# Kernel tuning notes

Hardware: AMD Instinct MI355X
Metric: run time of the kernel (lower is better)

The kernel has to match this reference:

```python
import jax, jax.numpy as jnp
import numpy as np

BSZ, L, H, P = 8, 4096, 512, 256  # batch, seq len, features, complex state dim (conj_sym)
DT_MIN, DT_MAX = 1e-3, 1e-1


def setup_inputs() -> dict:
    key = jax.random.key(0)
    k_u, k_B, k_C, k_D, k_dt = jax.random.split(key, 5)
    u = jax.random.normal(k_u, (BSZ, L, H), dtype=jnp.float32)
    # HiPPO-like stable init for the diagonal state matrix
    Lambda_re = -0.5 * jnp.ones((P,), dtype=jnp.float32)
    Lambda_im = jnp.pi * jnp.arange(P, dtype=jnp.float32)
    # lecun-normal-ish scaling for real/imag parts of B (fan_in = H) and C (fan_in = P)
    B = jax.random.normal(k_B, (P, H, 2), dtype=jnp.float32) / jnp.sqrt(2.0 * H)
    C = jax.random.normal(k_C, (H, P, 2), dtype=jnp.float32) / jnp.sqrt(2.0 * P)
    D = jax.random.normal(k_D, (H,), dtype=jnp.float32)
    log_step = jax.random.uniform(k_dt, (P, 1), dtype=jnp.float32,
                                  minval=jnp.log(DT_MIN), maxval=jnp.log(DT_MAX))
    return {"u": u, "Lambda_re": Lambda_re, "Lambda_im": Lambda_im,
            "B": B, "C": C, "D": D, "log_step": log_step}


def _binop(q_i, q_j):
    """Associative binary operator for diagonal linear recurrence."""
    A_i, b_i = q_i
    A_j, b_j = q_j
    return (A_j * A_i, A_j * b_i + b_j)


def reference(u, Lambda_re, Lambda_im, B, C, D, log_step):
    # --- setup / discretization (zero-order hold) ---
    Lambda = (Lambda_re + 1j * Lambda_im).astype(jnp.complex64)      # (P,)
    B_tilde = (B[..., 0] + 1j * B[..., 1]).astype(jnp.complex64)     # (P,H)
    C_tilde = (C[..., 0] + 1j * C[..., 1]).astype(jnp.complex64)     # (H,P)
    step = jnp.exp(log_step[:, 0])                                   # (P,)
    Lambda_bar = jnp.exp(Lambda * step)                              # (P,)
    B_bar = ((Lambda_bar - 1.0) / Lambda)[:, None] * B_tilde         # (P,H)

    # --- parallel scan over the sequence (diagonal SSM) ---
    Bu = jnp.einsum('blh,ph->blp', u, B_bar)                         # (B,L,P) complex64
    Lam = jnp.broadcast_to(Lambda_bar, Bu.shape)                     # (B,L,P)
    _, xs = jax.lax.associative_scan(_binop, (Lam, Bu), axis=1)      # (B,L,P)

    # --- emissions (factor 2 from conjugate symmetry) + feedthrough ---
    ys = 2.0 * jnp.einsum('blp,hp->blh', xs, C_tilde).real + D * u   # (B,L,H)
    return jax.nn.gelu(ys)
```

## Files before the change

kernel.cpp:

```cpp
#include <hip/hip_runtime.h>
#include <cstdint>
#include <cstddef>

typedef unsigned short u16;
typedef short short8 __attribute__((ext_vector_type(8)));
typedef float floatx4 __attribute__((ext_vector_type(4)));

#define DEVINL __device__ __forceinline__

static constexpr int BSZ = 8, SEQL = 4096, H = 512, P = 256;
static constexpr int M = BSZ * SEQL;
static constexpr int KD = 512;
static constexpr int ND = 512;
static constexpr int CHUNK = 32;
static constexpr int NCH = SEQL / CHUNK;

DEVINL u16 f2bf(float f) {
  union { float f; unsigned u; } v; v.f = f;
  unsigned r = (v.u + 0x7fffu + ((v.u >> 16) & 1u)) >> 16;
  return (u16)r;
}
DEVINL float bf2f(u16 h) {
  union { unsigned u; float f; } v; v.u = ((unsigned)h) << 16; return v.f;
}

DEVINL void gload_lds16(const u16* g, u16* l) {
  __builtin_amdgcn_global_load_lds(
      (const __attribute__((address_space(1))) unsigned*)g,
      (__attribute__((address_space(3))) unsigned*)l, 16, 0, 0);
}

__global__ void setup_kernel(const float* __restrict__ Lre, const float* __restrict__ Lim,
                             const float* __restrict__ logstep,
                             float2* __restrict__ lam, float2* __restrict__ ffac) {
  int p = threadIdx.x;
  if (p >= P) return;
  float lr = Lre[p], li = Lim[p];
  float st = expf(logstep[p]);
  float mag = expf(lr * st);
  float ang = li * st;
  float cr = mag * cosf(ang);
  float ci = mag * sinf(ang);
  lam[p] = make_float2(cr, ci);
  float a = cr - 1.0f, b = ci;
  float den = lr * lr + li * li;
  float fr = (a * lr + b * li) / den;
  float fi = (b * lr - a * li) / den;
  ffac[p] = make_float2(fr, fi);
}

__global__ void bt1_kernel(const float2* __restrict__ Bin,
                           const float2* __restrict__ ffac,
                           u16* __restrict__ bt1) {
  int idx = blockIdx.x * 256 + threadIdx.x;
  int p = idx / H, h = idx % H;
  float2 bv = Bin[(size_t)p * H + h];
  float2 f = ffac[p];
  float br = f.x * bv.x - f.y * bv.y;
  float bi = f.x * bv.y + f.y * bv.x;
  bt1[(size_t)(2 * p) * H + h]     = f2bf(br);
  bt1[(size_t)(2 * p + 1) * H + h] = f2bf(bi);
}

__global__ void bt2_kernel(const float* __restrict__ Cin, u16* __restrict__ bt2) {
  int idx = blockIdx.x * 256 + threadIdx.x;
  float c = Cin[idx];
  float v = (idx & 1) ? -2.0f * c : 2.0f * c;
  bt2[idx] = f2bf(v);
}

__global__ void ucvt_kernel(const float4* __restrict__ uin, ushort4* __restrict__ ubf) {
  int idx = blockIdx.x * 256 + threadIdx.x;
  float4 f = uin[idx];
  ushort4 o;
  o.x = f2bf(f.x); o.y = f2bf(f.y); o.z = f2bf(f.z); o.w = f2bf(f.w);
  ubf[idx] = o;
}

template <int MODE>
__global__ __launch_bounds__(256, 2) void gemm_bt(const u16* __restrict__ A,
                                                  const u16* __restrict__ Bt,
                                                  u16* __restrict__ outBf,
                                                  float* __restrict__ outF,
                                                  const float* __restrict__ Dv,
                                                  const u16* __restrict__ ubf) {
  __shared__ u16 As[3][128 * 32];
  __shared__ u16 Bs[3][256 * 32];
  const int tid = threadIdx.x;

  const int hw = blockIdx.x;
  const int logical = (hw & 7) * 64 + (hw >> 3);
  const int bm = logical >> 1;
  const int bn = logical & 1;

  const int wave = tid >> 6, lane = tid & 63;
  const int quad = lane >> 4, l16 = lane & 15;
  const int wm = (wave & 1) << 6;
  const int wn = (wave >> 1) << 7;

  floatx4 acc[4][8] = {};

  const u16* Ab = A + (size_t)bm * 128 * KD;
  const u16* Bb = Bt + (size_t)bn * 256 * KD;
  const int srow = tid >> 2;
  const int scol = (tid & 3) << 3;

#define STAGE(buf, kofs)                                                                   \
  do {                                                                                     \
    gload_lds16(Ab + (size_t)srow * KD + (kofs) + scol,         &As[buf][tid * 8]);        \
    gload_lds16(Ab + (size_t)(srow + 64) * KD + (kofs) + scol,  &As[buf][2048 + tid * 8]); \
    gload_lds16(Bb + (size_t)srow * KD + (kofs) + scol,         &Bs[buf][tid * 8]);        \
    gload_lds16(Bb + (size_t)(srow + 64) * KD + (kofs) + scol,  &Bs[buf][2048 + tid * 8]); \
    gload_lds16(Bb + (size_t)(srow + 128) * KD + (kofs) + scol, &Bs[buf][4096 + tid * 8]); \
    gload_lds16(Bb + (size_t)(srow + 192) * KD + (kofs) + scol, &Bs[buf][6144 + tid * 8]); \
  } while (0)

  STAGE(0, 0);
  STAGE(1, 32);
  asm volatile("s_waitcnt vmcnt(6)" ::: "memory");
  __builtin_amdgcn_sched_barrier(0);
  __builtin_amdgcn_s_barrier();
  __builtin_amdgcn_sched_barrier(0);

  constexpr int NK = KD / 32;
#pragma unroll
  for (int ks = 0; ks < NK; ks++) {
    const int k0 = ks * 32;
    const int cur = ks % 3;

    if (ks + 2 < NK) STAGE((ks + 2) % 3, k0 + 64);

    short8 af[4], bfr[8];
#pragma unroll
    for (int t = 0; t < 4; t++)
      af[t] = *(const short8*)&As[cur][(wm + t * 16 + l16) * 32 + quad * 8];
#pragma unroll
    for (int t = 0; t < 8; t++)
      bfr[t] = *(const short8*)&Bs[cur][(wn + t * 16 + l16) * 32 + quad * 8];

    asm volatile("s_waitcnt lgkmcnt(0)" ::: "memory");
    __builtin_amdgcn_sched_barrier(0);

    __builtin_amdgcn_s_setprio(1);
#pragma unroll
    for (int tm = 0; tm < 4; tm++)
#pragma unroll
      for (int tn = 0; tn < 8; tn++)
        acc[tm][tn] = __builtin_amdgcn_mfma_f32_16x16x32_bf16(af[tm], bfr[tn], acc[tm][tn], 0, 0, 0);
    __builtin_amdgcn_s_setprio(0);

    if (ks + 2 < NK) {
      asm volatile("s_waitcnt vmcnt(6)" ::: "memory");
      __builtin_amdgcn_sched_barrier(0);
      __builtin_amdgcn_s_barrier();
      __builtin_amdgcn_sched_barrier(0);
    } else if (ks + 1 < NK) {
      asm volatile("s_waitcnt vmcnt(0)" ::: "memory");
      __builtin_amdgcn_sched_barrier(0);
      __builtin_amdgcn_s_barrier();
      __builtin_amdgcn_sched_barrier(0);
    }
  }
#undef STAGE

  const int row_base = bm * 128 + wm + quad * 4;
  const int col_base = bn * 256 + wn + l16;
  float dv[8];
  if (MODE == 1) {
#pragma unroll
    for (int tn = 0; tn < 8; tn++) dv[tn] = Dv[col_base + tn * 16];
  }
#pragma unroll
  for (int tm = 0; tm < 4; tm++) {
#pragma unroll
    for (int tn = 0; tn < 8; tn++) {
      int n = col_base + tn * 16;
#pragma unroll
      for (int r = 0; r < 4; r++) {
        int m = row_base + tm * 16 + r;
        float v = acc[tm][tn][r];
        if (MODE == 0) {
          outBf[(size_t)m * ND + n] = f2bf(v);
        } else {
          float uv = bf2f(ubf[(size_t)m * ND + n]);
          float ys = v + dv[tn] * uv;
          float zz = ys + 0.044715f * (ys * ys * ys);
          float e = __builtin_amdgcn_exp2f(-2.3022082f * zz);
          outF[(size_t)m * ND + n] = ys * __builtin_amdgcn_rcpf(1.0f + e);
        }
      }
    }
  }
}

__global__ __launch_bounds__(256) void scan_carry(const u16* __restrict__ Bu,
                                                  const float2* __restrict__ lam,
                                                  float2* __restrict__ carry) {
  int p = threadIdx.x;
  int c = blockIdx.x;
  int b = blockIdx.y;
  float2 lm = lam[p];
  float xr = 0.f, xi = 0.f;
  const u16* base = Bu + ((size_t)b * SEQL + (size_t)c * CHUNK) * 512 + 2 * p;
  for (int l = 0; l < CHUNK; l++) {
    unsigned w = *(const unsigned*)(base + (size_t)l * 512);
    float br = bf2f((u16)(w & 0xffffu));
    float bi = bf2f((u16)(w >> 16));
    float nr = lm.x * xr - lm.y * xi + br;
    float ni = lm.x * xi + lm.y * xr + bi;
    xr = nr; xi = ni;
  }
  carry[((size_t)b * NCH + c) * P + p] = make_float2(xr, xi);
}

__global__ __launch_bounds__(256) void scan_prefix(const float2* __restrict__ carry,
                                                   const float2* __restrict__ lam,
                                                   float2* __restrict__ prefix) {
  int p = threadIdx.x;
  int b = blockIdx.x;
  float2 lm = lam[p];
  float ar = lm.x, ai = lm.y;
  for (int i = 0; i < 5; i++) { float nr = ar * ar - ai * ai, ni = 2.f * ar * ai; ar = nr; ai = ni; }
  float pr = 0.f, pi = 0.f;
  for (int c = 0; c < NCH; c++) {
    prefix[((size_t)b * NCH + c) * P + p] = make_float2(pr, pi);
    float2 ca = carry[((size_t)b * NCH + c) * P + p];
    float nr = ar * pr - ai * pi + ca.x;
    float ni = ar * pi + ai * pr + ca.y;
    pr = nr; pi = ni;
  }
}

__global__ __launch_bounds__(256) void scan_apply(u16* __restrict__ Bu,
                                                  const float2* __restrict__ lam,
                                                  const float2* __restrict__ prefix) {
  int p = threadIdx.x;
  int c = blockIdx.x;
  int b = blockIdx.y;
  float2 lm = lam[p];
  float2 pf = prefix[((size_t)b * NCH + c) * P + p];
  float xr = pf.x, xi = pf.y;
  u16* base = Bu + ((size_t)b * SEQL + (size_t)c * CHUNK) * 512 + 2 * p;
  for (int l = 0; l < CHUNK; l++) {
    unsigned* addr = (unsigned*)(base + (size_t)l * 512);
    unsigned w = *addr;
    float br = bf2f((u16)(w & 0xffffu));
    float bi = bf2f((u16)(w >> 16));
    float nr = lm.x * xr - lm.y * xi + br;
    float ni = lm.x * xi + lm.y * xr + bi;
    xr = nr; xi = ni;
    *addr = (unsigned)f2bf(nr) | ((unsigned)f2bf(ni) << 16);
  }
}

extern "C" void kernel_launch(void* const* d_in, const int* in_sizes, int n_in,
                              void* d_out, int out_size, void* d_ws, size_t ws_size,
                              hipStream_t stream) {
  const float* u      = (const float*)d_in[0];
  const float* Lre    = (const float*)d_in[1];
  const float* Lim    = (const float*)d_in[2];
  const float* Bin    = (const float*)d_in[3];
  const float* Cin    = (const float*)d_in[4];
  const float* Dv     = (const float*)d_in[5];
  const float* lstep  = (const float*)d_in[6];
  float* out          = (float*)d_out;

  char* ws = (char*)d_ws;
  float2* lam    = (float2*)(ws + 0);
  float2* ffac   = (float2*)(ws + 2048);
  u16*    bt1    = (u16*)   (ws + 4096);
  u16*    bt2    = (u16*)   (ws + 528384);
  u16*    ubf    = (u16*)   (ws + 1052672);
  u16*    Bu     = (u16*)   (ws + 34607104);
  float2* carry  = (float2*)(ws + 68161536);
  float2* prefix = (float2*)(ws + 69210112);

  setup_kernel<<<1, 256, 0, stream>>>(Lre, Lim, lstep, lam, ffac);
  bt1_kernel<<<(P * H) / 256, 256, 0, stream>>>((const float2*)Bin, ffac, bt1);
  bt2_kernel<<<(H * P * 2) / 256, 256, 0, stream>>>(Cin, bt2);
  ucvt_kernel<<<(M * H / 4) / 256, 256, 0, stream>>>((const float4*)u, (ushort4*)ubf);

  gemm_bt<0><<<(M / 128) * (ND / 256), 256, 0, stream>>>(ubf, bt1, Bu, nullptr, nullptr, nullptr);

  scan_carry <<<dim3(NCH, BSZ), 256, 0, stream>>>(Bu, lam, carry);
  scan_prefix<<<BSZ, 256, 0, stream>>>(carry, lam, prefix);
  scan_apply <<<dim3(NCH, BSZ), 256, 0, stream>>>(Bu, lam, prefix);

  gemm_bt<1><<<(M / 128) * (ND / 256), 256, 0, stream>>>(Bu, bt2, nullptr, out, Dv, ubf);
}
```

Measured before the change: 205.7 us.

## Fuse fp32-to-bf16 conversion into GEMM A-load and merge scan prefix into apply

The first GEMM now reads fp32 u directly into registers, converts to bf16 and writes to LDS, which removes the separate ucvt kernel and its bf16 workspace round trip. The second GEMM reads fp32 u for the feedthrough term instead of the bf16 copy. The scan_prefix kernel is removed: each scan_apply block recomputes its chunk prefix serially from the carries. That trades one small launch for redundant work that grows with chunk index, up to 128 steps. The register-staged A path adds VGPR pressure and doubles the A global traffic bytes inside the GEMM.

```diff
diff --git a/kernel.cpp b/kernel.cpp
--- a/kernel.cpp
+++ b/kernel.cpp
@@ -69,21 +69,14 @@
   bt2[idx] = f2bf(v);
 }
 
-__global__ void ucvt_kernel(const float4* __restrict__ uin, ushort4* __restrict__ ubf) {
-  int idx = blockIdx.x * 256 + threadIdx.x;
-  float4 f = uin[idx];
-  ushort4 o;
-  o.x = f2bf(f.x); o.y = f2bf(f.y); o.z = f2bf(f.z); o.w = f2bf(f.w);
-  ubf[idx] = o;
-}
-
 template <int MODE>
 __global__ __launch_bounds__(256, 2) void gemm_bt(const u16* __restrict__ A,
+                                                  const float* __restrict__ Af32,
                                                   const u16* __restrict__ Bt,
                                                   u16* __restrict__ outBf,
                                                   float* __restrict__ outF,
                                                   const float* __restrict__ Dv,
-                                                  const u16* __restrict__ ubf) {
+                                                  const float* __restrict__ U32) {
   __shared__ u16 As[3][128 * 32];
   __shared__ u16 Bs[3][256 * 32];
   const int tid = threadIdx.x;
@@ -100,35 +93,96 @@
 
   floatx4 acc[4][8] = {};
 
-  const u16* Ab = A + (size_t)bm * 128 * KD;
-  const u16* Bb = Bt + (size_t)bn * 256 * KD;
+  const u16*   Ab  = (MODE == 0) ? nullptr : A + (size_t)bm * 128 * KD;
+  const float* Afb = (MODE == 0) ? Af32 + (size_t)bm * 128 * KD : nullptr;
+  const u16*   Bb  = Bt + (size_t)bn * 256 * KD;
   const int srow = tid >> 2;
   const int scol = (tid & 3) << 3;
 
-#define STAGE(buf, kofs)                                                                   \
+  float4 aR[2][4];
+
+#define STAGE_B(buf, kofs)                                                                 \
   do {                                                                                     \
-    gload_lds16(Ab + (size_t)srow * KD + (kofs) + scol,         &As[buf][tid * 8]);        \
-    gload_lds16(Ab + (size_t)(srow + 64) * KD + (kofs) + scol,  &As[buf][2048 + tid * 8]); \
     gload_lds16(Bb + (size_t)srow * KD + (kofs) + scol,         &Bs[buf][tid * 8]);        \
     gload_lds16(Bb + (size_t)(srow + 64) * KD + (kofs) + scol,  &Bs[buf][2048 + tid * 8]); \
     gload_lds16(Bb + (size_t)(srow + 128) * KD + (kofs) + scol, &Bs[buf][4096 + tid * 8]); \
     gload_lds16(Bb + (size_t)(srow + 192) * KD + (kofs) + scol, &Bs[buf][6144 + tid * 8]); \
   } while (0)
 
-  STAGE(0, 0);
-  STAGE(1, 32);
-  asm volatile("s_waitcnt vmcnt(6)" ::: "memory");
-  __builtin_amdgcn_sched_barrier(0);
-  __builtin_amdgcn_s_barrier();
-  __builtin_amdgcn_sched_barrier(0);
+#define STAGE_A_LDS(buf, kofs)                                                             \
+  do {                                                                                     \
+    gload_lds16(Ab + (size_t)srow * KD + (kofs) + scol,        &As[buf][tid * 8]);         \
+    gload_lds16(Ab + (size_t)(srow + 64) * KD + (kofs) + scol, &As[buf][2048 + tid * 8]);  \
+  } while (0)
+
+#define ISSUE_A(set, kofs)                                                                 \
+  do {                                                                                     \
+    aR[set][0] = *(const float4*)(Afb + (size_t)srow * KD + (kofs) + scol);                \
+    aR[set][1] = *(const float4*)(Afb + (size_t)srow * KD + (kofs) + scol + 4);            \
+    aR[set][2] = *(const float4*)(Afb + (size_t)(srow + 64) * KD + (kofs) + scol);         \
+    aR[set][3] = *(const float4*)(Afb + (size_t)(srow + 64) * KD + (kofs) + scol + 4);     \
+  } while (0)
+
+#define WRITE_A(set, buf)                                                                  \
+  do {                                                                                     \
+    short8 w0, w1;                                                                         \
+    w0[0] = (short)f2bf(aR[set][0].x); w0[1] = (short)f2bf(aR[set][0].y);                  \
+    w0[2] = (short)f2bf(aR[set][0].z); w0[3] = (short)f2bf(aR[set][0].w);                  \
+    w0[4] = (short)f2bf(aR[set][1].x); w0[5] = (short)f2bf(aR[set][1].y);                  \
+    w0[6] = (short)f2bf(aR[set][1].z); w0[7] = (short)f2bf(aR[set][1].w);                  \
+    w1[0] = (short)f2bf(aR[set][2].x); w1[1] = (short)f2bf(aR[set][2].y);                  \
+    w1[2] = (short)f2bf(aR[set][2].z); w1[3] = (short)f2bf(aR[set][2].w);                  \
+    w1[4] = (short)f2bf(aR[set][3].x); w1[5] = (short)f2bf(aR[set][3].y);                  \
+    w1[6] = (short)f2bf(aR[set][3].z); w1[7] = (short)f2bf(aR[set][3].w);                  \
+    *(short8*)&As[buf][tid * 8]        = w0;                                               \
+    *(short8*)&As[buf][2048 + tid * 8] = w1;                                               \
+  } while (0)
+
+#define VMW(n) asm volatile("s_waitcnt vmcnt(" #n ")" ::: "memory");                       \
+               __builtin_amdgcn_sched_barrier(0)
+#define LGKW   asm volatile("s_waitcnt lgkmcnt(0)" ::: "memory");                          \
+               __builtin_amdgcn_sched_barrier(0)
+#define BARR   __builtin_amdgcn_s_barrier();                                               \
+               __builtin_amdgcn_sched_barrier(0)
 
   constexpr int NK = KD / 32;
+
+  if constexpr (MODE == 0) {
+    ISSUE_A(0, 0);
+    STAGE_B(0, 0);
+    ISSUE_A(1, 32);
+    STAGE_B(1, 32);
+    VMW(12);
+    WRITE_A(0, 0);
+    VMW(8);
+    LGKW;
+    BARR;
+  } else {
+    STAGE_A_LDS(0, 0);
+    STAGE_B(0, 0);
+    STAGE_A_LDS(1, 32);
+    STAGE_B(1, 32);
+    VMW(6);
+    BARR;
+  }
+
 #pragma unroll
   for (int ks = 0; ks < NK; ks++) {
     const int k0 = ks * 32;
     const int cur = ks % 3;
-
-    if (ks + 2 < NK) STAGE((ks + 2) % 3, k0 + 64);
+    const bool issue = (ks + 2 < NK);
+
+    if constexpr (MODE == 0) {
+      if (issue) {
+        ISSUE_A(ks & 1, k0 + 64);
+        STAGE_B((ks + 2) % 3, k0 + 64);
+      }
+    } else {
+      if (issue) {
+        STAGE_A_LDS((ks + 2) % 3, k0 + 64);
+        STAGE_B((ks + 2) % 3, k0 + 64);
+      }
+    }
 
     short8 af[4], bfr[8];
 #pragma unroll
@@ -138,8 +192,14 @@
     for (int t = 0; t < 8; t++)
       bfr[t] = *(const short8*)&Bs[cur][(wn + t * 16 + l16) * 32 + quad * 8];
 
-    asm volatile("s_waitcnt lgkmcnt(0)" ::: "memory");
-    __builtin_amdgcn_sched_barrier(0);
+    if constexpr (MODE == 0) {
+      if (ks + 1 < NK) {
+        if (issue) { VMW(12); } else { VMW(4); }
+        WRITE_A((ks + 1) & 1, (ks + 1) % 3);
+      }
+    }
+
+    LGKW;
 
     __builtin_amdgcn_s_setprio(1);
 #pragma unroll
@@ -149,19 +209,22 @@
         acc[tm][tn] = __builtin_amdgcn_mfma_f32_16x16x32_bf16(af[tm], bfr[tn], acc[tm][tn], 0, 0, 0);
     __builtin_amdgcn_s_setprio(0);
 
-    if (ks + 2 < NK) {
-      asm volatile("s_waitcnt vmcnt(6)" ::: "memory");
-      __builtin_amdgcn_sched_barrier(0);
-      __builtin_amdgcn_s_barrier();
-      __builtin_amdgcn_sched_barrier(0);
-    } else if (ks + 1 < NK) {
-      asm volatile("s_waitcnt vmcnt(0)" ::: "memory");
-      __builtin_amdgcn_sched_barrier(0);
-      __builtin_amdgcn_s_barrier();
-      __builtin_amdgcn_sched_barrier(0);
+    if (ks + 1 < NK) {
+      if constexpr (MODE == 0) {
+        if (issue) { VMW(8); } else { VMW(0); }
+      } else {
+        if (issue) { VMW(6); } else { VMW(0); }
+      }
+      BARR;
     }
   }
-#undef STAGE
+#undef STAGE_B
+#undef STAGE_A_LDS
+#undef ISSUE_A
+#undef WRITE_A
+#undef VMW
+#undef LGKW
+#undef BARR
 
   const int row_base = bm * 128 + wm + quad * 4;
   const int col_base = bn * 256 + wn + l16;
@@ -182,7 +245,7 @@
         if (MODE == 0) {
           outBf[(size_t)m * ND + n] = f2bf(v);
         } else {
-          float uv = bf2f(ubf[(size_t)m * ND + n]);
+          float uv = U32[(size_t)m * ND + n];
           float ys = v + dv[tn] * uv;
           float zz = ys + 0.044715f * (ys * ys * ys);
           float e = __builtin_amdgcn_exp2f(-2.3022082f * zz);
@@ -213,33 +276,23 @@
   carry[((size_t)b * NCH + c) * P + p] = make_float2(xr, xi);
 }
 
-__global__ __launch_bounds__(256) void scan_prefix(const float2* __restrict__ carry,
-                                                   const float2* __restrict__ lam,
-                                                   float2* __restrict__ prefix) {
+__global__ __launch_bounds__(256) void scan_apply(u16* __restrict__ Bu,
+                                                  const float2* __restrict__ lam,
+                                                  const float2* __restrict__ carry) {
   int p = threadIdx.x;
-  int b = blockIdx.x;
+  int c = blockIdx.x;
+  int b = blockIdx.y;
   float2 lm = lam[p];
   float ar = lm.x, ai = lm.y;
   for (int i = 0; i < 5; i++) { float nr = ar * ar - ai * ai, ni = 2.f * ar * ai; ar = nr; ai = ni; }
   float pr = 0.f, pi = 0.f;
-  for (int c = 0; c < NCH; c++) {
-    prefix[((size_t)b * NCH + c) * P + p] = make_float2(pr, pi);
-    float2 ca = carry[((size_t)b * NCH + c) * P + p];
+  for (int j = 0; j < c; j++) {
+    float2 ca = carry[((size_t)b * NCH + j) * P + p];
     float nr = ar * pr - ai * pi + ca.x;
     float ni = ar * pi + ai * pr + ca.y;
     pr = nr; pi = ni;
   }
-}
-
-__global__ __launch_bounds__(256) void scan_apply(u16* __restrict__ Bu,
-                                                  const float2* __restrict__ lam,
-                                                  const float2* __restrict__ prefix) {
-  int p = threadIdx.x;
-  int c = blockIdx.x;
-  int b = blockIdx.y;
-  float2 lm = lam[p];
-  float2 pf = prefix[((size_t)b * NCH + c) * P + p];
-  float xr = pf.x, xi = pf.y;
+  float xr = pr, xi = pi;
   u16* base = Bu + ((size_t)b * SEQL + (size_t)c * CHUNK) * 512 + 2 * p;
   for (int l = 0; l < CHUNK; l++) {
     unsigned* addr = (unsigned*)(base + (size_t)l * 512);
@@ -270,21 +323,17 @@
   float2* ffac   = (float2*)(ws + 2048);
   u16*    bt1    = (u16*)   (ws + 4096);
   u16*    bt2    = (u16*)   (ws + 528384);
-  u16*    ubf    = (u16*)   (ws + 1052672);
-  u16*    Bu     = (u16*)   (ws + 34607104);
-  float2* carry  = (float2*)(ws + 68161536);
-  float2* prefix = (float2*)(ws + 69210112);
+  u16*    Bu     = (u16*)   (ws + 1052672);
+  float2* carry  = (float2*)(ws + 34607104);
 
   setup_kernel<<<1, 256, 0, stream>>>(Lre, Lim, lstep, lam, ffac);
   bt1_kernel<<<(P * H) / 256, 256, 0, stream>>>((const float2*)Bin, ffac, bt1);
   bt2_kernel<<<(H * P * 2) / 256, 256, 0, stream>>>(Cin, bt2);
-  ucvt_kernel<<<(M * H / 4) / 256, 256, 0, stream>>>((const float4*)u, (ushort4*)ubf);
-
-  gemm_bt<0><<<(M / 128) * (ND / 256), 256, 0, stream>>>(ubf, bt1, Bu, nullptr, nullptr, nullptr);
+
+  gemm_bt<0><<<(M / 128) * (ND / 256), 256, 0, stream>>>(nullptr, u, bt1, Bu, nullptr, nullptr, nullptr);
 
   scan_carry <<<dim3(NCH, BSZ), 256, 0, stream>>>(Bu, lam, carry);
-  scan_prefix<<<BSZ, 256, 0, stream>>>(carry, lam, prefix);
-  scan_apply <<<dim3(NCH, BSZ), 256, 0, stream>>>(Bu, lam, prefix);
-
-  gemm_bt<1><<<(M / 128) * (ND / 256), 256, 0, stream>>>(Bu, bt2, nullptr, out, Dv, ubf);
-}
+  scan_apply <<<dim3(NCH, BSZ), 256, 0, stream>>>(Bu, lam, carry);
+
+  gemm_bt<1><<<(M / 128) * (ND / 256), 256, 0, stream>>>(Bu, nullptr, bt2, nullptr, out, Dv, u);
+}
```

Measured after the change: 230.7 us. +12.2%, slower.
